# Optimization experiments

Measured on AMD Instinct MI355X. Metric: run time of the kernel, lower is better.

Reference implementation:

```python
import jax, jax.numpy as jnp
import numpy as np

B, T, D = 8, 4096, 256
GATE_MIN, GATE_MAX = 0.01, 0.99


def setup_inputs() -> dict:
    key = jax.random.key(0)
    ks = jax.random.split(key, 8)
    inp = {
        "x_re": jax.random.normal(ks[0], (B, T, D), jnp.float32),
        "x_im": jax.random.normal(ks[1], (B, T, D), jnp.float32),
        "s0_re": jnp.zeros((B, D), jnp.float32),
        "s0_im": jnp.zeros((B, D), jnp.float32),
        "decay_re": jax.random.normal(ks[2], (D,), jnp.float32),
        "decay_im": 0.1 * jax.random.normal(ks[3], (D,), jnp.float32),
        "Wm": 0.02 * jax.random.normal(ks[4], (2 * D, 2 * D), jnp.float32)
              + jnp.eye(2 * D, dtype=jnp.float32),  # eye_ init on diag blocks
        "bm": jnp.zeros((2 * D,), jnp.float32),
        "Wo": 0.02 * jax.random.normal(ks[5], (2 * D, 2 * D), jnp.float32),
        "bo": jnp.zeros((2 * D,), jnp.float32),
        "Wg": 0.02 * jax.random.normal(ks[6], (D, 2 * D), jnp.float32),
        "bg": jnp.zeros((D,), jnp.float32),
    }
    return inp


def reference(x_re, x_im, s0_re, s0_im, decay_re, decay_im,
              Wm, bm, Wo, bo, Wg, bg):
    # decay = sigmoid(decay_re) + i*decay_im
    dr = jax.nn.sigmoid(decay_re)
    di = decay_im

    # scan over time: inputs as [T, B, D]
    xs = (jnp.swapaxes(x_re, 0, 1), jnp.swapaxes(x_im, 0, 1))

    def step(carry, xt):
        s_re, s_im = carry
        xr, xi = xt                                   # [B, D]
        x_cat = jnp.concatenate([xr, xi], axis=-1)    # [B, 2D]
        x_in = x_cat @ Wm.T + bm
        ur, ui = jnp.split(x_in, 2, axis=-1)
        # complex mul-add: new_state = prev_state * decay + update
        ns_re = s_re * dr - s_im * di + ur
        ns_im = s_re * di + s_im * dr + ui
        s_cat = jnp.concatenate([ns_re, ns_im], axis=-1)  # [B, 2D]
        source = s_cat @ Wo.T + bo                        # [B, 2D] (re|im)
        gate = jnp.clip(jax.nn.sigmoid(s_cat @ Wg.T + bg), GATE_MIN, GATE_MAX)
        y = jnp.concatenate([source, gate], axis=-1)      # [B, 3D]
        return (ns_re, ns_im), y

    _, ys = jax.lax.scan(step, (s0_re, s0_im), xs)        # [T, B, 3D]
    return jnp.swapaxes(ys, 0, 1)                          # [B, T, 3D] = [src_re|src_im|gate]
```

## Files before the change

kernel.cpp:

```cpp
#include <hip/hip_runtime.h>
#include <hip/hip_bf16.h>
#include <cstdint>
#include <cstddef>


typedef __bf16 bf16;
typedef __bf16 bf16x4 __attribute__((ext_vector_type(4)));
typedef __bf16 bf16x8 __attribute__((ext_vector_type(8)));
typedef float floatx4 __attribute__((ext_vector_type(4)));

#define NB 8
#define NT 4096
#define ND 256
#define BT (NB * NT)
#define TWOD 512
#define CHUNK 128
#define NCHUNK (NT / CHUNK)

static __device__ __forceinline__ float sigmoidf_(float x) {
  return 1.0f / (1.0f + __expf(-x));
}

static __device__ __forceinline__ void async_copy16(const void* g, void* l) {
  __builtin_amdgcn_global_load_lds(
      (__attribute__((address_space(1))) void*)g,
      (__attribute__((address_space(3))) void*)l, 16, 0, 0);
}


__global__ void k_convert_x(const float* __restrict__ xr,
                            const float* __restrict__ xi,
                            bf16* __restrict__ X) {
  const int idx = (blockIdx.x * 256 + threadIdx.x) * 4;
  const int row = idx >> 8;
  const int dd = idx & 255;
  const float4 vr = *(const float4*)(xr + idx);
  const float4 vi = *(const float4*)(xi + idx);
  bf16x4 br, bi;
  br[0] = (bf16)vr.x; br[1] = (bf16)vr.y; br[2] = (bf16)vr.z; br[3] = (bf16)vr.w;
  bi[0] = (bf16)vi.x; bi[1] = (bf16)vi.y; bi[2] = (bf16)vi.z; bi[3] = (bf16)vi.w;
  *(bf16x4*)(X + (size_t)row * TWOD + dd) = br;
  *(bf16x4*)(X + (size_t)row * TWOD + ND + dd) = bi;
}

__global__ void k_prep_weights(const float* __restrict__ Wm,
                               const float* __restrict__ Wo,
                               const float* __restrict__ Wg,
                               const float* __restrict__ bo,
                               const float* __restrict__ bg,
                               bf16* __restrict__ Wm_b,
                               bf16* __restrict__ Wc_b,
                               float* __restrict__ bc) {
  const int i = blockIdx.x * 256 + threadIdx.x;
  Wm_b[i] = (bf16)Wm[i];
  Wc_b[i] = (bf16)Wo[i];
  if (i < 131072) Wc_b[262144 + i] = (bf16)Wg[i];
  if (i < 512) bc[i] = bo[i];
  if (i < 256) bc[512 + i] = bg[i];
}

template <int MODE>
__global__ __launch_bounds__(256, 2) void gemm_bt(
    const bf16* __restrict__ A, const bf16* __restrict__ Bw,
    const float* __restrict__ bias, void* __restrict__ Cout,
    const int K, const int N, const int actStart) {
  __shared__ __align__(16) bf16 As[128 * 32];
  __shared__ __align__(16) bf16 Bs[128 * 32];
  const int tid = threadIdx.x;
  const int wave = tid >> 6;
  const int lane = tid & 63;
  const int quad = lane >> 4;
  const int l16 = lane & 15;
  const int m0 = blockIdx.y * 128;
  const int n0 = blockIdx.x * 128;
  const int wm = (wave >> 1) * 64;
  const int wn = (wave & 1) * 64;

  floatx4 acc[4][4];
#pragma unroll
  for (int i = 0; i < 4; ++i)
#pragma unroll
    for (int j = 0; j < 4; ++j) acc[i][j] = (floatx4)0.0f;

  for (int k0 = 0; k0 < K; k0 += 32) {
    __syncthreads();
#pragma unroll
    for (int i = 0; i < 2; ++i) {
      const int seg = i * 4 + wave;
      const int f = seg * 512 + lane * 8;
      const int row = f >> 5;
      const int kk = f & 31;
      async_copy16(A + (size_t)(m0 + row) * K + (k0 + kk), As + seg * 512);
      async_copy16(Bw + (size_t)(n0 + row) * K + (k0 + kk), Bs + seg * 512);
    }
    __syncthreads();

    bf16x8 af[4], bfr[4];
#pragma unroll
    for (int mi = 0; mi < 4; ++mi)
      af[mi] = *(const bf16x8*)(As + (wm + mi * 16 + l16) * 32 + quad * 8);
#pragma unroll
    for (int ni = 0; ni < 4; ++ni)
      bfr[ni] = *(const bf16x8*)(Bs + (wn + ni * 16 + l16) * 32 + quad * 8);
#pragma unroll
    for (int mi = 0; mi < 4; ++mi)
#pragma unroll
      for (int ni = 0; ni < 4; ++ni)
        acc[mi][ni] = __builtin_amdgcn_mfma_f32_16x16x32_bf16(
            af[mi], bfr[ni], acc[mi][ni], 0, 0, 0);
  }

#pragma unroll
  for (int mi = 0; mi < 4; ++mi) {
    const int rb = m0 + wm + mi * 16 + quad * 4;
#pragma unroll
    for (int ni = 0; ni < 4; ++ni) {
      const int col = n0 + wn + ni * 16 + l16;
      const float bb = bias[col];
      if (MODE == 0) {
        bf16* C = (bf16*)Cout;
#pragma unroll
        for (int r = 0; r < 4; ++r)
          C[(size_t)(rb + r) * N + col] = (bf16)(acc[mi][ni][r] + bb);
      } else {
        float* C = (float*)Cout;
#pragma unroll
        for (int r = 0; r < 4; ++r) {
          float v = acc[mi][ni][r] + bb;
          if (col >= actStart) v = fminf(fmaxf(sigmoidf_(v), 0.01f), 0.99f);
          C[(size_t)(rb + r) * N + col] = v;
        }
      }
    }
  }
}

__global__ void k_scan_pass1(const bf16* __restrict__ U,
                             const float* __restrict__ decay_re,
                             const float* __restrict__ decay_im,
                             float* __restrict__ Fre, float* __restrict__ Fim) {
  const int d = threadIdx.x;
  const int c = blockIdx.x;
  const int b = blockIdx.y;
  const float dr = sigmoidf_(decay_re[d]);
  const float di = decay_im[d];
  float sr = 0.f, si = 0.f;
  const size_t rowbase = (size_t)b * NT + (size_t)c * CHUNK;
  const bf16* Ur = U + rowbase * TWOD + d;
#pragma unroll 4
  for (int j = 0; j < CHUNK; ++j) {
    const float ur = (float)Ur[(size_t)j * TWOD];
    const float ui = (float)Ur[(size_t)j * TWOD + ND];
    const float nr = sr * dr - si * di + ur;
    const float ni = sr * di + si * dr + ui;
    sr = nr; si = ni;
  }
  const int o = (b * NCHUNK + c) * ND + d;
  Fre[o] = sr; Fim[o] = si;
}

__global__ void k_scan_pass2(const float* __restrict__ Fre,
                             const float* __restrict__ Fim,
                             const float* __restrict__ s0_re,
                             const float* __restrict__ s0_im,
                             const float* __restrict__ decay_re,
                             const float* __restrict__ decay_im,
                             float* __restrict__ Ire, float* __restrict__ Iim) {
  const int d = threadIdx.x;
  const int b = blockIdx.x;
  const float dr = sigmoidf_(decay_re[d]);
  const float di = decay_im[d];
  float pr = dr, pi = di;
#pragma unroll
  for (int i = 0; i < 7; ++i) {
    const float nr = pr * pr - pi * pi;
    const float ni = 2.f * pr * pi;
    pr = nr; pi = ni;
  }
  float sr = s0_re[b * ND + d];
  float si = s0_im[b * ND + d];
  for (int c = 0; c < NCHUNK; ++c) {
    const int o = (b * NCHUNK + c) * ND + d;
    Ire[o] = sr; Iim[o] = si;
    const float nr = sr * pr - si * pi + Fre[o];
    const float ni = sr * pi + si * pr + Fim[o];
    sr = nr; si = ni;
  }
}

__global__ void k_scan_pass3(bf16* __restrict__ U,
                             const float* __restrict__ decay_re,
                             const float* __restrict__ decay_im,
                             const float* __restrict__ Ire,
                             const float* __restrict__ Iim) {
  const int d = threadIdx.x;
  const int c = blockIdx.x;
  const int b = blockIdx.y;
  const float dr = sigmoidf_(decay_re[d]);
  const float di = decay_im[d];
  const int o = (b * NCHUNK + c) * ND + d;
  float sr = Ire[o], si = Iim[o];
  const size_t rowbase = (size_t)b * NT + (size_t)c * CHUNK;
  bf16* Ur = U + rowbase * TWOD + d;
#pragma unroll 4
  for (int j = 0; j < CHUNK; ++j) {
    const float ur = (float)Ur[(size_t)j * TWOD];
    const float ui = (float)Ur[(size_t)j * TWOD + ND];
    const float nr = sr * dr - si * di + ur;
    const float ni = sr * di + si * dr + ui;
    sr = nr; si = ni;
    Ur[(size_t)j * TWOD] = (bf16)nr;
    Ur[(size_t)j * TWOD + ND] = (bf16)ni;
  }
}


extern "C" void kernel_launch(void* const* d_in, const int* in_sizes, int n_in,
                              void* d_out, int out_size, void* d_ws, size_t ws_size,
                              hipStream_t stream) {
  const float* x_re = (const float*)d_in[0];
  const float* x_im = (const float*)d_in[1];
  const float* s0_re = (const float*)d_in[2];
  const float* s0_im = (const float*)d_in[3];
  const float* decay_re = (const float*)d_in[4];
  const float* decay_im = (const float*)d_in[5];
  const float* Wm = (const float*)d_in[6];
  const float* bm = (const float*)d_in[7];
  const float* Wo = (const float*)d_in[8];
  const float* bo = (const float*)d_in[9];
  const float* Wg = (const float*)d_in[10];
  const float* bg = (const float*)d_in[11];

  char* ws = (char*)d_ws;
  const size_t XCAT_OFF = 0;
  const size_t U_OFF = 33554432;
  const size_t WM_OFF = 67108864;
  const size_t WC_OFF = WM_OFF + 524288;
  const size_t BC_OFF = WC_OFF + 786432;
  const size_t FRE_OFF = BC_OFF + 4096;
  const size_t FIM_OFF = FRE_OFF + 262144;
  const size_t IRE_OFF = FIM_OFF + 262144;
  const size_t IIM_OFF = IRE_OFF + 262144;

  bf16* Xcat = (bf16*)(ws + XCAT_OFF);
  bf16* U = (bf16*)(ws + U_OFF);
  bf16* Wm_b = (bf16*)(ws + WM_OFF);
  bf16* Wc_b = (bf16*)(ws + WC_OFF);
  float* bc = (float*)(ws + BC_OFF);
  float* Fre = (float*)(ws + FRE_OFF);
  float* Fim = (float*)(ws + FIM_OFF);
  float* Ire = (float*)(ws + IRE_OFF);
  float* Iim = (float*)(ws + IIM_OFF);

  float* out = (float*)d_out;

  k_convert_x<<<dim3(8192), 256, 0, stream>>>(x_re, x_im, Xcat);
  k_prep_weights<<<dim3(1024), 256, 0, stream>>>(Wm, Wo, Wg, bo, bg, Wm_b, Wc_b, bc);
  gemm_bt<0><<<dim3(4, 256), 256, 0, stream>>>(Xcat, Wm_b, bm, U, 512, 512, 0);
  k_scan_pass1<<<dim3(NCHUNK, NB), ND, 0, stream>>>(U, decay_re, decay_im, Fre, Fim);
  k_scan_pass2<<<dim3(NB), ND, 0, stream>>>(Fre, Fim, s0_re, s0_im, decay_re, decay_im, Ire, Iim);
  k_scan_pass3<<<dim3(NCHUNK, NB), ND, 0, stream>>>(U, decay_re, decay_im, Ire, Iim);
  gemm_bt<1><<<dim3(6, 256), 256, 0, stream>>>(U, Wc_b, bc, d_out, 512, 768, 512);
}
```

Before: 286.0 us.

## Merge prep kernels, widen GEMM K-tile to 64 with XOR-swizzled LDS, swap grid axes

Fuses the input conversion and weight conversion into one launch, removing a kernel launch. The GEMM now stages 64-wide K tiles with an XOR swizzle on LDS chunks to avoid bank conflicts, halving the number of barrier pairs per tile. Grid axes are swapped so consecutive blocks walk along M, and the occupancy hint in launch_bounds is dropped. Doubled LDS usage may reduce blocks per CU.

```diff
diff --git a/kernel.cpp b/kernel.cpp
--- a/kernel.cpp
+++ b/kernel.cpp
@@ -27,87 +27,98 @@
       (__attribute__((address_space(3))) void*)l, 16, 0, 0);
 }
 
-
-__global__ void k_convert_x(const float* __restrict__ xr,
-                            const float* __restrict__ xi,
-                            bf16* __restrict__ X) {
-  const int idx = (blockIdx.x * 256 + threadIdx.x) * 4;
-  const int row = idx >> 8;
-  const int dd = idx & 255;
-  const float4 vr = *(const float4*)(xr + idx);
-  const float4 vi = *(const float4*)(xi + idx);
-  bf16x4 br, bi;
-  br[0] = (bf16)vr.x; br[1] = (bf16)vr.y; br[2] = (bf16)vr.z; br[3] = (bf16)vr.w;
-  bi[0] = (bf16)vi.x; bi[1] = (bf16)vi.y; bi[2] = (bf16)vi.z; bi[3] = (bf16)vi.w;
-  *(bf16x4*)(X + (size_t)row * TWOD + dd) = br;
-  *(bf16x4*)(X + (size_t)row * TWOD + ND + dd) = bi;
-}
-
-__global__ void k_prep_weights(const float* __restrict__ Wm,
-                               const float* __restrict__ Wo,
-                               const float* __restrict__ Wg,
-                               const float* __restrict__ bo,
-                               const float* __restrict__ bg,
-                               bf16* __restrict__ Wm_b,
-                               bf16* __restrict__ Wc_b,
-                               float* __restrict__ bc) {
-  const int i = blockIdx.x * 256 + threadIdx.x;
-  Wm_b[i] = (bf16)Wm[i];
-  Wc_b[i] = (bf16)Wo[i];
-  if (i < 131072) Wc_b[262144 + i] = (bf16)Wg[i];
-  if (i < 512) bc[i] = bo[i];
-  if (i < 256) bc[512 + i] = bg[i];
+__global__ void k_prep(const float* __restrict__ xr,
+                       const float* __restrict__ xi,
+                       const float* __restrict__ Wm,
+                       const float* __restrict__ Wo,
+                       const float* __restrict__ Wg,
+                       const float* __restrict__ bo,
+                       const float* __restrict__ bg,
+                       bf16* __restrict__ X,
+                       bf16* __restrict__ Wm_b,
+                       bf16* __restrict__ Wc_b,
+                       float* __restrict__ bc) {
+  const int bid = blockIdx.x;
+  if (bid < 8192) {
+    const int idx = (bid * 256 + threadIdx.x) * 4;
+    const int row = idx >> 8;
+    const int dd = idx & 255;
+    const float4 vr = *(const float4*)(xr + idx);
+    const float4 vi = *(const float4*)(xi + idx);
+    bf16x4 br, bi;
+    br[0] = (bf16)vr.x; br[1] = (bf16)vr.y; br[2] = (bf16)vr.z; br[3] = (bf16)vr.w;
+    bi[0] = (bf16)vi.x; bi[1] = (bf16)vi.y; bi[2] = (bf16)vi.z; bi[3] = (bf16)vi.w;
+    *(bf16x4*)(X + (size_t)row * TWOD + dd) = br;
+    *(bf16x4*)(X + (size_t)row * TWOD + ND + dd) = bi;
+  } else {
+    const int i = (bid - 8192) * 256 + threadIdx.x;
+    Wm_b[i] = (bf16)Wm[i];
+    Wc_b[i] = (bf16)Wo[i];
+    if (i < 131072) Wc_b[262144 + i] = (bf16)Wg[i];
+    if (i < 512) bc[i] = bo[i];
+    if (i < 256) bc[512 + i] = bg[i];
+  }
 }
 
 template <int MODE>
-__global__ __launch_bounds__(256, 2) void gemm_bt(
+__global__ __launch_bounds__(256) void gemm_bt(
     const bf16* __restrict__ A, const bf16* __restrict__ Bw,
     const float* __restrict__ bias, void* __restrict__ Cout,
     const int K, const int N, const int actStart) {
-  __shared__ __align__(16) bf16 As[128 * 32];
-  __shared__ __align__(16) bf16 Bs[128 * 32];
+  __shared__ __align__(16) bf16 As[128 * 64];
+  __shared__ __align__(16) bf16 Bs[128 * 64];
   const int tid = threadIdx.x;
   const int wave = tid >> 6;
   const int lane = tid & 63;
   const int quad = lane >> 4;
   const int l16 = lane & 15;
-  const int m0 = blockIdx.y * 128;
-  const int n0 = blockIdx.x * 128;
+  const int m0 = blockIdx.x * 128;
+  const int n0 = blockIdx.y * 128;
   const int wm = (wave >> 1) * 64;
   const int wn = (wave & 1) * 64;
 
+  const int srow = lane >> 3;
+  const int schunk = (lane & 7) ^ (srow & 7);
+
   floatx4 acc[4][4];
 #pragma unroll
   for (int i = 0; i < 4; ++i)
 #pragma unroll
     for (int j = 0; j < 4; ++j) acc[i][j] = (floatx4)0.0f;
 
-  for (int k0 = 0; k0 < K; k0 += 32) {
+  for (int k0 = 0; k0 < K; k0 += 64) {
     __syncthreads();
 #pragma unroll
-    for (int i = 0; i < 2; ++i) {
-      const int seg = i * 4 + wave;
-      const int f = seg * 512 + lane * 8;
-      const int row = f >> 5;
-      const int kk = f & 31;
-      async_copy16(A + (size_t)(m0 + row) * K + (k0 + kk), As + seg * 512);
-      async_copy16(Bw + (size_t)(n0 + row) * K + (k0 + kk), Bs + seg * 512);
+    for (int i = 0; i < 4; ++i) {
+      const int seg = wave * 4 + i;
+      const int row = seg * 8 + srow;
+      async_copy16(A + (size_t)(m0 + row) * K + k0 + schunk * 8, As + seg * 512);
+      async_copy16(Bw + (size_t)(n0 + row) * K + k0 + schunk * 8, Bs + seg * 512);
     }
     __syncthreads();
 
-    bf16x8 af[4], bfr[4];
-#pragma unroll
-    for (int mi = 0; mi < 4; ++mi)
-      af[mi] = *(const bf16x8*)(As + (wm + mi * 16 + l16) * 32 + quad * 8);
-#pragma unroll
-    for (int ni = 0; ni < 4; ++ni)
-      bfr[ni] = *(const bf16x8*)(Bs + (wn + ni * 16 + l16) * 32 + quad * 8);
-#pragma unroll
-    for (int mi = 0; mi < 4; ++mi)
-#pragma unroll
-      for (int ni = 0; ni < 4; ++ni)
-        acc[mi][ni] = __builtin_amdgcn_mfma_f32_16x16x32_bf16(
-            af[mi], bfr[ni], acc[mi][ni], 0, 0, 0);
+#pragma unroll
+    for (int s = 0; s < 2; ++s) {
+      bf16x8 af[4], bfr[4];
+#pragma unroll
+      for (int mi = 0; mi < 4; ++mi) {
+        const int row = wm + mi * 16 + l16;
+        const int ch = ((s << 2) | quad) ^ (l16 & 7);
+        af[mi] = *(const bf16x8*)(As + row * 64 + ch * 8);
+      }
+#pragma unroll
+      for (int ni = 0; ni < 4; ++ni) {
+        const int row = wn + ni * 16 + l16;
+        const int ch = ((s << 2) | quad) ^ (l16 & 7);
+        bfr[ni] = *(const bf16x8*)(Bs + row * 64 + ch * 8);
+      }
+#pragma unroll
+      for (int mi = 0; mi < 4; ++mi)
+#pragma unroll
+        for (int ni = 0; ni < 4; ++ni)
+          acc[mi][ni] = __builtin_amdgcn_mfma_f32_16x16x32_bf16(
+              af[mi], bfr[ni], acc[mi][ni], 0, 0, 0);
+    }
   }
 
 #pragma unroll
@@ -252,13 +263,11 @@
   float* Ire = (float*)(ws + IRE_OFF);
   float* Iim = (float*)(ws + IIM_OFF);
 
-  float* out = (float*)d_out;
-
-  k_convert_x<<<dim3(8192), 256, 0, stream>>>(x_re, x_im, Xcat);
-  k_prep_weights<<<dim3(1024), 256, 0, stream>>>(Wm, Wo, Wg, bo, bg, Wm_b, Wc_b, bc);
-  gemm_bt<0><<<dim3(4, 256), 256, 0, stream>>>(Xcat, Wm_b, bm, U, 512, 512, 0);
+  k_prep<<<dim3(9216), 256, 0, stream>>>(x_re, x_im, Wm, Wo, Wg, bo, bg,
+                                         Xcat, Wm_b, Wc_b, bc);
+  gemm_bt<0><<<dim3(256, 4), 256, 0, stream>>>(Xcat, Wm_b, bm, U, 512, 512, 0);
   k_scan_pass1<<<dim3(NCHUNK, NB), ND, 0, stream>>>(U, decay_re, decay_im, Fre, Fim);
   k_scan_pass2<<<dim3(NB), ND, 0, stream>>>(Fre, Fim, s0_re, s0_im, decay_re, decay_im, Ire, Iim);
   k_scan_pass3<<<dim3(NCHUNK, NB), ND, 0, stream>>>(U, decay_re, decay_im, Ire, Iim);
-  gemm_bt<1><<<dim3(6, 256), 256, 0, stream>>>(U, Wc_b, bc, d_out, 512, 768, 512);
-}
+  gemm_bt<1><<<dim3(256, 6), 256, 0, stream>>>(U, Wc_b, bc, d_out, 512, 768, 512);
+}
```

New measurement: 266.5 us. 6.8% less time.
